# Kernel optimization log

Hardware: AMD Instinct MI355X
Metric: run time of the kernel (lower is better)

Reference implementation:

```python
import jax, jax.numpy as jnp
import numpy as np

B, N, D = 2, 2048, 256
H, HID, EN = 8, 64, 2
ALPHA = 0.2
NEG = -9e15


def setup_inputs() -> dict:
    key = jax.random.key(0)
    k1, k2, k3, k4, k5, k6 = jax.random.split(key, 6)
    fea_mats = jax.random.normal(k1, (B, N, D), dtype=jnp.float32)
    adj_mats = jax.random.randint(k2, (B, N, N), 0, 2).astype(jnp.float32)
    # xavier-uniform-like init (gain 1.414)
    def xav(k, shape):
        fan_in, fan_out = shape[-2], shape[-1]
        bound = 1.414 * np.sqrt(6.0 / (fan_in + fan_out))
        return jax.random.uniform(k, shape, jnp.float32, -bound, bound)
    W_att = xav(k3, (H, D, HID))          # per-head projection
    a_att = xav(k4, (H, 2 * HID, 1))      # per-head attention vector
    W_last = xav(k5, (H * HID, EN))       # last-layer projection
    a_last = xav(k6, (2 * EN, 1))         # last-layer attention vector
    return {"fea_mats": fea_mats, "adj_mats": adj_mats,
            "W_att": W_att, "a_att": a_att,
            "W_last": W_last, "a_last": a_last}


def _leaky(x):
    return jnp.where(x >= 0, x, ALPHA * x)


def _masked_attn(e, adj):
    # torch: where(adj!=0, e, 0) * adj; masked_fill(==0, -9e15); softmax(dim=1 over columns)
    att = jnp.where(adj != 0, e, jnp.zeros_like(e)) * adj
    att = jnp.where(att == 0, jnp.full_like(att, NEG), att)
    return jax.nn.softmax(att, axis=-1)


def reference(fea_mats, adj_mats, W_att, a_att, W_last, a_last):
    # ---- multi-head GAT layers (concat=True), eval mode -> dropout = identity ----
    wh = jnp.einsum('bnd,hdo->bhno', fea_mats, W_att)        # [B,H,N,HID]
    a1 = a_att[:, :HID, 0]                                   # [H,HID]
    a2 = a_att[:, HID:, 0]                                   # [H,HID]
    e1 = jnp.einsum('bhno,ho->bhn', wh, a1)                  # regulon part
    e2 = jnp.einsum('bhno,ho->bhn', wh, a2)                  # gene part
    e = _leaky(e1[:, :, :, None] + e2[:, :, None, :])        # [B,H,N,N]
    att = _masked_attn(e, adj_mats[:, None])                 # [B,H,N,N]
    x = jax.nn.elu(jnp.einsum('bhnm,bhmo->bhno', att, wh))   # [B,H,N,HID]
    x = jnp.transpose(x, (0, 2, 1, 3)).reshape(B, N, H * HID)
    # ---- last layer (concat=False), adj narrowed to square (already square) ----
    wh2 = jnp.einsum('bnd,de->bne', x, W_last)               # [B,N,EN]
    b1 = a_last[:EN, 0]
    b2 = a_last[EN:, 0]
    e = _leaky(jnp.einsum('bne,e->bn', wh2, b1)[:, :, None]
               + jnp.einsum('bne,e->bn', wh2, b2)[:, None, :])  # [B,N,N]
    att = _masked_attn(e, adj_mats)
    out = jax.nn.elu(jnp.einsum('bnm,bme->bne', att, wh2))   # [B,N,EN]
    return out
```

## Files before the change

### kernel.cpp

```cpp
#include <hip/hip_runtime.h>
#include <hip/hip_bf16.h>
#include <cstdint>
#include <cstddef>

#define B_ 2
#define N_ 2048
#define D_ 256
#define H_ 8
#define HID_ 64
#define EN_ 2
#define ALPHA 0.2f
#define NEGBIG (-3.0e38f)
#define LOG2E 1.4426950408889634f

typedef __bf16 bf16x8 __attribute__((ext_vector_type(8)));
typedef float f32x4 __attribute__((ext_vector_type(4)));
typedef unsigned short ushort8 __attribute__((ext_vector_type(8)));
typedef float float4v __attribute__((ext_vector_type(4)));
typedef float float2v __attribute__((ext_vector_type(2)));
typedef unsigned int uint2v __attribute__((ext_vector_type(2)));
typedef unsigned int uint4v __attribute__((ext_vector_type(4)));

__device__ __forceinline__ unsigned short f2bf(float f) {
    unsigned int u = __builtin_bit_cast(unsigned int, f);
    unsigned int r = u + 0x7FFFu + ((u >> 16) & 1u);
    return (unsigned short)(r >> 16);
}
__device__ __forceinline__ float bf2f(unsigned short u) {
    unsigned int x = ((unsigned int)u) << 16;
    return __builtin_bit_cast(float, x);
}
__device__ __forceinline__ float leakyf(float x) { return fmaxf(x, ALPHA * x); }
__device__ __forceinline__ float ub(unsigned int d, int e) {
    return (float)((d >> (8 * e)) & 0xffu);
}

__device__ __forceinline__ ushort8 cvt8(const float* __restrict__ p) {
    float4v x0 = *(const float4v*)p;
    float4v x1 = *(const float4v*)(p + 4);
    ushort8 r;
    #pragma unroll
    for (int e = 0; e < 4; ++e) { r[e] = f2bf(x0[e]); r[e + 4] = f2bf(x1[e]); }
    return r;
}

__global__ __launch_bounds__(256) void k_prep(const float* __restrict__ adj,
                                              unsigned char* __restrict__ adj8) {
    size_t base = ((size_t)blockIdx.x * 256 + threadIdx.x) * 8;
    float4v a = *(const float4v*)(adj + base);
    float4v b = *(const float4v*)(adj + base + 4);
    unsigned int lo = 0, hi = 0;
    #pragma unroll
    for (int e = 0; e < 4; ++e) {
        lo |= (a[e] != 0.f ? 1u : 0u) << (8 * e);
        hi |= (b[e] != 0.f ? 1u : 0u) << (8 * e);
    }
    uint2v o; o[0] = lo; o[1] = hi;
    *(uint2v*)(adj8 + base) = o;
}

__global__ void k_transpose_w(const float* __restrict__ W,
                              unsigned short* __restrict__ WT) {
    int h = blockIdx.x;
    const float* Wh = W + (size_t)h * D_ * HID_;
    unsigned short* WTh = WT + (size_t)h * HID_ * D_;
    for (int idx = threadIdx.x; idx < D_ * HID_; idx += blockDim.x) {
        int d = idx / HID_, o = idx % HID_;
        WTh[o * D_ + d] = f2bf(Wh[idx]);
    }
}

__global__ __launch_bounds__(256) void k_wh(
    const float* __restrict__ fea,
    const unsigned short* __restrict__ WT,
    const float* __restrict__ a_att,
    unsigned short* __restrict__ whT,
    float* __restrict__ e1, float* __restrict__ e2)
{
    int i0 = blockIdx.x << 6;
    int h0 = blockIdx.y * 2;
    int b  = blockIdx.z;

    __shared__ __align__(16) union SmemA {
        struct { unsigned short fa[64 * 72]; unsigned short wt[2][64 * 72]; } s;
        float tr[64 * 65];
    } u;

    int t = threadIdx.x;
    int lane = t & 63;
    int wv = t >> 6;
    int hw = wv & 1;
    int half = wv >> 1;
    int r = lane & 15, q = lane >> 4;
    int ra = t >> 2;
    int cc = (t & 3) * 16;
    int rowbase = half * 32;

    f32x4 acc[2][4] = {};

    const float* fearow = fea + ((size_t)(b * N_ + i0 + ra)) * D_;
    const unsigned short* wt0row = WT + ((size_t)(h0 * 64 + ra)) * D_;
    const unsigned short* wt1row = WT + ((size_t)((h0 + 1) * 64 + ra)) * D_;

    for (int d0 = 0; d0 < D_; d0 += 64) {
        *(ushort8*)&u.s.fa[ra * 72 + cc]       = cvt8(fearow + d0 + cc);
        *(ushort8*)&u.s.fa[ra * 72 + cc + 8]   = cvt8(fearow + d0 + cc + 8);
        *(ushort8*)&u.s.wt[0][ra * 72 + cc]     = *(const ushort8*)(wt0row + d0 + cc);
        *(ushort8*)&u.s.wt[0][ra * 72 + cc + 8] = *(const ushort8*)(wt0row + d0 + cc + 8);
        *(ushort8*)&u.s.wt[1][ra * 72 + cc]     = *(const ushort8*)(wt1row + d0 + cc);
        *(ushort8*)&u.s.wt[1][ra * 72 + cc + 8] = *(const ushort8*)(wt1row + d0 + cc + 8);
        __syncthreads();
        #pragma unroll
        for (int k0 = 0; k0 < 64; k0 += 32) {
            bf16x8 a0 = *(const bf16x8*)&u.s.fa[(rowbase + r) * 72 + k0 + q * 8];
            bf16x8 a1 = *(const bf16x8*)&u.s.fa[(rowbase + 16 + r) * 72 + k0 + q * 8];
            #pragma unroll
            for (int f = 0; f < 4; ++f) {
                bf16x8 bb = *(const bf16x8*)&u.s.wt[hw][(16 * f + r) * 72 + k0 + q * 8];
                acc[0][f] = __builtin_amdgcn_mfma_f32_16x16x32_bf16(a0, bb, acc[0][f], 0, 0, 0);
                acc[1][f] = __builtin_amdgcn_mfma_f32_16x16x32_bf16(a1, bb, acc[1][f], 0, 0, 0);
            }
        }
        __syncthreads();
    }

    float a1v[4], a2v[4];
    #pragma unroll
    for (int f = 0; f < 4; ++f) {
        a1v[f] = a_att[(h0 + hw) * 128 + 16 * f + r];
        a2v[f] = a_att[(h0 + hw) * 128 + 64 + 16 * f + r];
    }
    #pragma unroll
    for (int m = 0; m < 2; ++m) {
        #pragma unroll
        for (int rr = 0; rr < 4; ++rr) {
            float s1 = 0.f, s2 = 0.f;
            #pragma unroll
            for (int f = 0; f < 4; ++f) { s1 += acc[m][f][rr] * a1v[f]; s2 += acc[m][f][rr] * a2v[f]; }
            #pragma unroll
            for (int sh = 1; sh < 16; sh <<= 1) {
                s1 += __shfl_xor(s1, sh, 64);
                s2 += __shfl_xor(s2, sh, 64);
            }
            if (r == 0) {
                int i = i0 + rowbase + 16 * m + 4 * q + rr;
                size_t idx = ((size_t)(b * H_ + h0 + hw)) * N_ + i;
                e1[idx] = s1 * LOG2E; e2[idx] = s2 * LOG2E;
            }
        }
    }

    #pragma unroll
    for (int hh = 0; hh < 2; ++hh) {
        __syncthreads();
        if (hw == hh) {
            #pragma unroll
            for (int m = 0; m < 2; ++m)
                #pragma unroll
                for (int f = 0; f < 4; ++f)
                    #pragma unroll
                    for (int rr = 0; rr < 4; ++rr)
                        u.tr[(16 * f + r) * 65 + rowbase + 16 * m + 4 * q + rr] = acc[m][f][rr];
        }
        __syncthreads();
        {
            int o = t >> 2;
            int ch = (t & 3) * 16;
            unsigned short tmp[16];
            #pragma unroll
            for (int e = 0; e < 16; ++e) tmp[e] = f2bf(u.tr[o * 65 + ch + e]);
            ushort8* dst = (ushort8*)(whT + (((size_t)(b * H_ + h0 + hh) * 64 + o)) * N_ + i0 + ch);
            dst[0] = *(ushort8*)&tmp[0];
            dst[1] = *(ushort8*)&tmp[8];
        }
    }
}

__global__ __launch_bounds__(256) void k_maxe2(const float* __restrict__ e2,
                                               float* __restrict__ mx) {
    int bh = blockIdx.x;
    int t = threadIdx.x;
    const float* row = e2 + (size_t)bh * N_;
    float M = NEGBIG;
    #pragma unroll
    for (int it = 0; it < N_ / 256; ++it) M = fmaxf(M, row[it * 256 + t]);
    #pragma unroll
    for (int s = 1; s < 64; s <<= 1) M = fmaxf(M, __shfl_xor(M, s, 64));
    __shared__ float red[4];
    if ((t & 63) == 0) red[t >> 6] = M;
    __syncthreads();
    if (t == 0) mx[bh] = fmaxf(fmaxf(red[0], red[1]), fmaxf(red[2], red[3]));
}

template<int JPER>
__global__ __launch_bounds__(512, 4) void k_pv2(
    const unsigned char* __restrict__ adj8,
    const unsigned short* __restrict__ whT,
    const float* __restrict__ e1g, const float* __restrict__ e2g,
    const float* __restrict__ maxE2,
    unsigned short* __restrict__ x_part,
    float* __restrict__ zPart)
{
    constexpr int NT = JPER / 64;
    int s  = blockIdx.x;
    int i0 = blockIdx.y << 7;
    int z  = blockIdx.z;
    int b  = z >> 2;
    int h0 = (z & 3) * 2;
    int bh0 = b * H_ + h0;
    int jBeg = s * JPER;

    __shared__ __align__(16) union {
        struct {
            unsigned short wt[2][2][4096];
            unsigned char  adjl[2][128 * 80];
            unsigned int   tv[2][JPER];
        } m;
        unsigned short epi[128][136];
    } u;

    int t = threadIdx.x;
    int lane = t & 63;
    int w = t >> 6;
    int hw = w & 1;
    int rw = (w >> 1) * 32;
    int r = lane & 15, q = lane >> 4;
    int bh = bh0 + hw;

    int ir0 = i0 + rw + r, ir1 = ir0 + 16;
    float mxv = maxE2[bh];
    float e1_0 = e1g[(size_t)bh * N_ + ir0];
    float e1_1 = e1g[(size_t)bh * N_ + ir1];
    float m0 = leakyf(e1_0 + mxv), m1 = leakyf(e1_1 + mxv);
    float sI0 = __builtin_amdgcn_exp2f(e1_0 - m0);
    float uI0 = __builtin_amdgcn_exp2f(ALPHA * e1_0 - m0);
    float sI1 = __builtin_amdgcn_exp2f(e1_1 - m1);
    float uI1 = __builtin_amdgcn_exp2f(ALPHA * e1_1 - m1);

    int sh = t >> 8;
    int so = (t & 255) >> 2;
    int sj = (t & 3) * 16;
    const unsigned short* wsrc = whT + ((size_t)(bh0 + sh) * 64 + so) * N_ + jBeg + sj;
    int wof0 = sh * 4096 + so * 64 + (sj ^ ((so & 7) << 3));
    int wof1 = sh * 4096 + so * 64 + ((sj + 8) ^ ((so & 7) << 3));
    int ar = t >> 2, ac = (t & 3) * 16;
    const unsigned char* asrc = adj8 + ((size_t)(b * N_ + i0 + ar)) * N_ + jBeg + ac;
    int aof = ar * 80 + ac;

    int swzr = (r & 7) << 3;
    int koff0 = (8 * q) ^ swzr;
    int koff1 = (32 + 8 * q) ^ swzr;

    bf16x8 ones;
    #pragma unroll
    for (int e = 0; e < 8; ++e) ones[e] = (__bf16)1.0f;

    f32x4 acc[2][4] = {};
    f32x4 accz[2] = {};

    ushort8 wA, wB;
    uint4v  aR;

#define LOADSTG(tile) do {                                        \
        wA = *(const ushort8*)(wsrc + (tile) * 64);               \
        wB = *(const ushort8*)(wsrc + (tile) * 64 + 8);           \
        aR = *(const uint4v*)(asrc + (tile) * 64);                \
    } while (0)

    for (int jj = t; jj < 2 * JPER; jj += 512) {
        int hh = jj >= JPER ? 1 : 0;
        int j = jj - hh * JPER;
        float ev = e2g[(size_t)(bh0 + hh) * N_ + jBeg + j];
        unsigned int pk = (unsigned int)f2bf(__builtin_amdgcn_exp2f(ev))
                        | ((unsigned int)f2bf(__builtin_amdgcn_exp2f(ALPHA * ev)) << 16);
        u.m.tv[hh][j] = pk;
    }
    LOADSTG(0);
    asm volatile("s_waitcnt vmcnt(0)" ::: "memory");
    *(ushort8*)((unsigned short*)u.m.wt[0] + wof0) = wA;
    *(ushort8*)((unsigned short*)u.m.wt[0] + wof1) = wB;
    *(uint4v*)&u.m.adjl[0][aof] = aR;
    if (NT > 1) LOADSTG(1);
    asm volatile("s_waitcnt lgkmcnt(0)" ::: "memory");
    __builtin_amdgcn_s_barrier();

    #pragma unroll 2
    for (int t8 = 0; t8 < NT; ++t8) {
        const int p = t8 & 1;
        if (t8 + 1 < NT) {
            asm volatile("s_waitcnt vmcnt(0)" ::: "memory");
            *(ushort8*)((unsigned short*)u.m.wt[p ^ 1] + wof0) = wA;
            *(ushort8*)((unsigned short*)u.m.wt[p ^ 1] + wof1) = wB;
            *(uint4v*)&u.m.adjl[p ^ 1][aof] = aR;
        }
        if (t8 + 2 < NT) LOADSTG(t8 + 2);

        const unsigned int* tvp = &u.m.tv[hw][t8 * 64 + q * 8];
        uint4v ta0 = *(const uint4v*)(tvp);
        uint4v ta1 = *(const uint4v*)(tvp + 4);
        uint4v tb0 = *(const uint4v*)(tvp + 32);
        uint4v tb1 = *(const uint4v*)(tvp + 36);
        const unsigned char* ab = &u.m.adjl[p][(rw + r) * 80 + q * 8];
        uint2v a0 = *(const uint2v*)(ab);
        uint2v a1 = *(const uint2v*)(ab + 32);
        uint2v a2 = *(const uint2v*)(ab + 16 * 80);
        uint2v a3 = *(const uint2v*)(ab + 16 * 80 + 32);

        bf16x8 pa00, pa01, pa10, pa11;
        #pragma unroll
        for (int e = 0; e < 4; ++e) {
            float tt, vv;
            unsigned int uu;
            uu = ta0[e];
            tt = __builtin_bit_cast(float, uu << 16);
            vv = __builtin_bit_cast(float, uu & 0xffff0000u);
            pa00[e] = (__bf16)(fmaxf(sI0 * tt, uI0 * vv) * ub(a0[0], e));
            pa10[e] = (__bf16)(fmaxf(sI1 * tt, uI1 * vv) * ub(a2[0], e));
            uu = ta1[e];
            tt = __builtin_bit_cast(float, uu << 16);
            vv = __builtin_bit_cast(float, uu & 0xffff0000u);
            pa00[e + 4] = (__bf16)(fmaxf(sI0 * tt, uI0 * vv) * ub(a0[1], e));
            pa10[e + 4] = (__bf16)(fmaxf(sI1 * tt, uI1 * vv) * ub(a2[1], e));
            uu = tb0[e];
            tt = __builtin_bit_cast(float, uu << 16);
            vv = __builtin_bit_cast(float, uu & 0xffff0000u);
            pa01[e] = (__bf16)(fmaxf(sI0 * tt, uI0 * vv) * ub(a1[0], e));
            pa11[e] = (__bf16)(fmaxf(sI1 * tt, uI1 * vv) * ub(a3[0], e));
            uu = tb1[e];
            tt = __builtin_bit_cast(float, uu << 16);
            vv = __builtin_bit_cast(float, uu & 0xffff0000u);
            pa01[e + 4] = (__bf16)(fmaxf(sI0 * tt, uI0 * vv) * ub(a1[1], e));
            pa11[e + 4] = (__bf16)(fmaxf(sI1 * tt, uI1 * vv) * ub(a3[1], e));
        }

        const unsigned short* Wb = (const unsigned short*)u.m.wt[p] + hw * 4096;
        bf16x8 bb;
        #pragma unroll
        for (int f = 0; f < 4; ++f) {
            bb = *(const bf16x8*)&Wb[f * 1024 + r * 64 + koff0];
            acc[0][f] = __builtin_amdgcn_mfma_f32_16x16x32_bf16(pa00, bb, acc[0][f], 0, 0, 0);
            acc[1][f] = __builtin_amdgcn_mfma_f32_16x16x32_bf16(pa10, bb, acc[1][f], 0, 0, 0);
        }
        accz[0] = __builtin_amdgcn_mfma_f32_16x16x32_bf16(pa00, ones, accz[0], 0, 0, 0);
        accz[1] = __builtin_amdgcn_mfma_f32_16x16x32_bf16(pa10, ones, accz[1], 0, 0, 0);
        #pragma unroll
        for (int f = 0; f < 4; ++f) {
            bb = *(const bf16x8*)&Wb[f * 1024 + r * 64 + koff1];
            acc[0][f] = __builtin_amdgcn_mfma_f32_16x16x32_bf16(pa01, bb, acc[0][f], 0, 0, 0);
            acc[1][f] = __builtin_amdgcn_mfma_f32_16x16x32_bf16(pa11, bb, acc[1][f], 0, 0, 0);
        }
        accz[0] = __builtin_amdgcn_mfma_f32_16x16x32_bf16(pa01, ones, accz[0], 0, 0, 0);
        accz[1] = __builtin_amdgcn_mfma_f32_16x16x32_bf16(pa11, ones, accz[1], 0, 0, 0);

        asm volatile("s_waitcnt lgkmcnt(0)" ::: "memory");
        __builtin_amdgcn_s_barrier();
    }
#undef LOADSTG

    if (r == 0) {
        #pragma unroll
        for (int mR = 0; mR < 2; ++mR)
            #pragma unroll
            for (int rr = 0; rr < 4; ++rr) {
                int i = i0 + rw + mR * 16 + 4 * q + rr;
                zPart[((size_t)(s * 16 + bh)) * N_ + i] = accz[mR][rr];
            }
    }

    #pragma unroll
    for (int mR = 0; mR < 2; ++mR)
        #pragma unroll
        for (int f = 0; f < 4; ++f)
            #pragma unroll
            for (int rr = 0; rr < 4; ++rr)
                u.epi[rw + mR * 16 + 4 * q + rr][hw * 64 + 16 * f + r] = f2bf(acc[mR][f][rr]);
    __syncthreads();
    {
        int tr = t >> 2;
        int ch = (t & 3) * 32;
        const ushort8* src = (const ushort8*)&u.epi[tr][ch];
        ushort8 v0 = src[0], v1 = src[1], v2 = src[2], v3 = src[3];
        unsigned short* dst = x_part
            + ((size_t)s * (B_ * N_) + (size_t)b * N_ + i0 + tr) * 512 + h0 * 64 + ch;
        ((ushort8*)dst)[0] = v0;
        ((ushort8*)dst)[1] = v1;
        ((ushort8*)dst)[2] = v2;
        ((ushort8*)dst)[3] = v3;
    }
}

__global__ __launch_bounds__(256) void k_wh2(
    const unsigned short* __restrict__ x_part,
    const float* __restrict__ zPart,
    const float* __restrict__ W_last,
    const float* __restrict__ a_last,
    float* __restrict__ wh2, float* __restrict__ g1, float* __restrict__ g2,
    int S)
{
    int idx = blockIdx.x * 4 + (threadIdx.x >> 6);
    int lane = threadIdx.x & 63;
    int b = idx >> 11, n = idx & (N_ - 1);
    float a0 = 0.f, a1 = 0.f;
    #pragma unroll
    for (int it = 0; it < 8; ++it) {
        int k = it * 64 + lane;
        float xv = 0.f, zv = 0.f;
        for (int s = 0; s < S; ++s) {
            xv += bf2f(x_part[((size_t)s * (B_ * N_) + idx) * 512 + k]);
            zv += zPart[((size_t)(s * 16 + b * 8 + it)) * N_ + n];
        }
        float x = (zv > 0.f) ? xv / zv : 0.f;
        x = x > 0.f ? x : expm1f(x);
        float2v wl = *(const float2v*)(W_last + k * 2);
        a0 += x * wl[0];
        a1 += x * wl[1];
    }
    #pragma unroll
    for (int s = 1; s < 64; s <<= 1) {
        a0 += __shfl_xor(a0, s, 64);
        a1 += __shfl_xor(a1, s, 64);
    }
    if (lane == 0) {
        wh2[idx * 2] = a0; wh2[idx * 2 + 1] = a1;
        g1[idx] = (a0 * a_last[0] + a1 * a_last[1]) * LOG2E;
        g2[idx] = (a0 * a_last[2] + a1 * a_last[3]) * LOG2E;
    }
}

__global__ __launch_bounds__(256) void k_out(
    const unsigned char* __restrict__ adj8,
    const float* __restrict__ wh2,
    const float* __restrict__ g1, const float* __restrict__ g2,
    float* __restrict__ out)
{
    int idx = blockIdx.x * 4 + (threadIdx.x >> 6);
    int lane = threadIdx.x & 63;
    int b = idx >> 11;
    float gi = g1[idx];
    const unsigned char* arow = adj8 + (size_t)idx * N_;
    const float* g2b = g2 + (size_t)b * N_;
    const float* wh2b = wh2 + (size_t)b * N_ * 2;

    float ep[32];
    float M = NEGBIG;
    #pragma unroll
    for (int it = 0; it < 8; ++it) {
        int j = it * 256 + lane * 4;
        unsigned int d = *(const unsigned int*)(arow + j);
        float4v s4 = *(const float4v*)(g2b + j);
        #pragma unroll
        for (int e = 0; e < 4; ++e) {
            float l = leakyf(gi + s4[e]);
            float v = ((d >> (8 * e)) & 0xffu) ? l : NEGBIG;
            ep[it * 4 + e] = v;
            M = fmaxf(M, v);
        }
    }
    #pragma unroll
    for (int s = 1; s < 64; s <<= 1) M = fmaxf(M, __shfl_xor(M, s, 64));

    float Z = 0.f, A0 = 0.f, A1 = 0.f;
    #pragma unroll
    for (int it = 0; it < 8; ++it) {
        int j = it * 256 + lane * 4;
        float4v wA = *(const float4v*)(wh2b + 2 * j);
        float4v wB = *(const float4v*)(wh2b + 2 * j + 4);
        #pragma unroll
        for (int e = 0; e < 4; ++e) {
            float p = __builtin_amdgcn_exp2f(ep[it * 4 + e] - M);
            Z += p;
            float w0 = (e < 2) ? wA[2 * e] : wB[2 * (e - 2)];
            float w1 = (e < 2) ? wA[2 * e + 1] : wB[2 * (e - 2) + 1];
            A0 += p * w0;
            A1 += p * w1;
        }
    }
    #pragma unroll
    for (int s = 1; s < 64; s <<= 1) {
        Z += __shfl_xor(Z, s, 64);
        A0 += __shfl_xor(A0, s, 64);
        A1 += __shfl_xor(A1, s, 64);
    }
    if (lane == 0) {
        float o0 = A0 / Z, o1 = A1 / Z;
        o0 = o0 > 0.f ? o0 : expm1f(o0);
        o1 = o1 > 0.f ? o1 : expm1f(o1);
        float2v ov; ov[0] = o0; ov[1] = o1;
        *(float2v*)(out + idx * 2) = ov;
    }
}

extern "C" void kernel_launch(void* const* d_in, const int* in_sizes, int n_in,
                              void* d_out, int out_size, void* d_ws, size_t ws_size,
                              hipStream_t stream) {
    const float* fea    = (const float*)d_in[0];
    const float* adj    = (const float*)d_in[1];
    const float* W_att  = (const float*)d_in[2];
    const float* a_att  = (const float*)d_in[3];
    const float* W_last = (const float*)d_in[4];
    const float* a_last = (const float*)d_in[5];

    char* ws = (char*)d_ws;
    float* e1  = (float*)(ws + 0);
    float* e2  = (float*)(ws + 131072);
    float* mxE = (float*)(ws + 262144);
    float* wh2 = (float*)(ws + 262400);
    float* g1  = (float*)(ws + 295168);
    float* g2  = (float*)(ws + 311552);
    unsigned short* WT  = (unsigned short*)(ws + 327936);
    unsigned short* whT = (unsigned short*)(ws + 590080);
    float* zPart = (float*)(ws + 4784384);
    unsigned char* adj8 = (unsigned char*)(ws + 5308672);
    unsigned short* x_part = (unsigned short*)(ws + 13697280);

    const size_t BASE = 13697280ULL, XPART = 4194304ULL;
    int S = (ws_size >= BASE + 2 * XPART) ? 2 : 1;

    k_prep<<<dim3(B_ * N_ * N_ / 2048), dim3(256), 0, stream>>>(adj, adj8);
    k_transpose_w<<<dim3(H_), dim3(256), 0, stream>>>(W_att, WT);
    k_wh<<<dim3(N_ / 64, H_ / 2, B_), dim3(256), 0, stream>>>(
        fea, WT, a_att, whT, e1, e2);
    k_maxe2<<<dim3(B_ * H_), dim3(256), 0, stream>>>(e2, mxE);
    if (S == 2)
        k_pv2<1024><<<dim3(2, N_ / 128, B_ * 4), dim3(512), 0, stream>>>(
            adj8, whT, e1, e2, mxE, x_part, zPart);
    else
        k_pv2<2048><<<dim3(1, N_ / 128, B_ * 4), dim3(512), 0, stream>>>(
            adj8, whT, e1, e2, mxE, x_part, zPart);
    k_wh2<<<dim3(B_ * N_ / 4), dim3(256), 0, stream>>>(
        x_part, zPart, W_last, a_last, wh2, g1, g2, S);
    k_out<<<dim3(B_ * N_ / 4), dim3(256), 0, stream>>>(
        adj8, wh2, g1, g2, (float*)d_out);
}
```

Before: 85.83 us.

## Fuse adjacency prep into projection kernel and compute e2 max via atomics

```diff
diff --git a/kernel.cpp b/kernel.cpp
--- a/kernel.cpp
+++ b/kernel.cpp
@@ -34,6 +34,14 @@
 __device__ __forceinline__ float ub(unsigned int d, int e) {
     return (float)((d >> (8 * e)) & 0xffu);
 }
+__device__ __forceinline__ unsigned fenc(float f) {
+    unsigned b = __builtin_bit_cast(unsigned, f);
+    return (b & 0x80000000u) ? ~b : (b | 0x80000000u);
+}
+__device__ __forceinline__ float fdec(unsigned k) {
+    unsigned b = (k & 0x80000000u) ? (k ^ 0x80000000u) : ~k;
+    return __builtin_bit_cast(float, b);
+}
 
 __device__ __forceinline__ ushort8 cvt8(const float* __restrict__ p) {
     float4v x0 = *(const float4v*)p;
@@ -44,24 +52,11 @@
     return r;
 }
 
-__global__ __launch_bounds__(256) void k_prep(const float* __restrict__ adj,
-                                              unsigned char* __restrict__ adj8) {
-    size_t base = ((size_t)blockIdx.x * 256 + threadIdx.x) * 8;
-    float4v a = *(const float4v*)(adj + base);
-    float4v b = *(const float4v*)(adj + base + 4);
-    unsigned int lo = 0, hi = 0;
-    #pragma unroll
-    for (int e = 0; e < 4; ++e) {
-        lo |= (a[e] != 0.f ? 1u : 0u) << (8 * e);
-        hi |= (b[e] != 0.f ? 1u : 0u) << (8 * e);
-    }
-    uint2v o; o[0] = lo; o[1] = hi;
-    *(uint2v*)(adj8 + base) = o;
-}
-
 __global__ void k_transpose_w(const float* __restrict__ W,
-                              unsigned short* __restrict__ WT) {
+                              unsigned short* __restrict__ WT,
+                              unsigned* __restrict__ mxE) {
     int h = blockIdx.x;
+    if (h == 0 && threadIdx.x < 16) mxE[threadIdx.x] = 0u;
     const float* Wh = W + (size_t)h * D_ * HID_;
     unsigned short* WTh = WT + (size_t)h * HID_ * D_;
     for (int idx = threadIdx.x; idx < D_ * HID_; idx += blockDim.x) {
@@ -70,21 +65,40 @@
     }
 }
 
-__global__ __launch_bounds__(256) void k_wh(
+#define PREP_BLOCKS 4096
+__global__ __launch_bounds__(256) void k_fused1(
+    const float* __restrict__ adj, unsigned char* __restrict__ adj8,
     const float* __restrict__ fea,
     const unsigned short* __restrict__ WT,
     const float* __restrict__ a_att,
     unsigned short* __restrict__ whT,
-    float* __restrict__ e1, float* __restrict__ e2)
+    float* __restrict__ e1, float* __restrict__ e2,
+    unsigned* __restrict__ mxE)
 {
-    int i0 = blockIdx.x << 6;
-    int h0 = blockIdx.y * 2;
-    int b  = blockIdx.z;
-
     __shared__ __align__(16) union SmemA {
         struct { unsigned short fa[64 * 72]; unsigned short wt[2][64 * 72]; } s;
         float tr[64 * 65];
     } u;
+
+    if (blockIdx.x < PREP_BLOCKS) {
+        size_t base = ((size_t)blockIdx.x * 256 + threadIdx.x) * 8;
+        float4v a = *(const float4v*)(adj + base);
+        float4v b = *(const float4v*)(adj + base + 4);
+        unsigned int lo = 0, hi = 0;
+        #pragma unroll
+        for (int e = 0; e < 4; ++e) {
+            lo |= (a[e] != 0.f ? 1u : 0u) << (8 * e);
+            hi |= (b[e] != 0.f ? 1u : 0u) << (8 * e);
+        }
+        uint2v o; o[0] = lo; o[1] = hi;
+        *(uint2v*)(adj8 + base) = o;
+        return;
+    }
+
+    int w = blockIdx.x - PREP_BLOCKS;
+    int i0 = (w & 31) << 6;
+    int h0 = ((w >> 5) & 3) * 2;
+    int b  = w >> 7;
 
     int t = threadIdx.x;
     int lane = t & 63;
@@ -130,6 +144,7 @@
         a1v[f] = a_att[(h0 + hw) * 128 + 16 * f + r];
         a2v[f] = a_att[(h0 + hw) * 128 + 64 + 16 * f + r];
     }
+    float ms2 = NEGBIG;
     #pragma unroll
     for (int m = 0; m < 2; ++m) {
         #pragma unroll
@@ -142,13 +157,18 @@
                 s1 += __shfl_xor(s1, sh, 64);
                 s2 += __shfl_xor(s2, sh, 64);
             }
+            float s2v = s2 * LOG2E;
+            ms2 = fmaxf(ms2, s2v);
             if (r == 0) {
                 int i = i0 + rowbase + 16 * m + 4 * q + rr;
                 size_t idx = ((size_t)(b * H_ + h0 + hw)) * N_ + i;
-                e1[idx] = s1 * LOG2E; e2[idx] = s2 * LOG2E;
+                e1[idx] = s1 * LOG2E; e2[idx] = s2v;
             }
         }
     }
+    ms2 = fmaxf(ms2, __shfl_xor(ms2, 16, 64));
+    ms2 = fmaxf(ms2, __shfl_xor(ms2, 32, 64));
+    if (lane == 0) atomicMax(&mxE[b * H_ + h0 + hw], fenc(ms2));
 
     #pragma unroll
     for (int hh = 0; hh < 2; ++hh) {
@@ -176,28 +196,12 @@
     }
 }
 
-__global__ __launch_bounds__(256) void k_maxe2(const float* __restrict__ e2,
-                                               float* __restrict__ mx) {
-    int bh = blockIdx.x;
-    int t = threadIdx.x;
-    const float* row = e2 + (size_t)bh * N_;
-    float M = NEGBIG;
-    #pragma unroll
-    for (int it = 0; it < N_ / 256; ++it) M = fmaxf(M, row[it * 256 + t]);
-    #pragma unroll
-    for (int s = 1; s < 64; s <<= 1) M = fmaxf(M, __shfl_xor(M, s, 64));
-    __shared__ float red[4];
-    if ((t & 63) == 0) red[t >> 6] = M;
-    __syncthreads();
-    if (t == 0) mx[bh] = fmaxf(fmaxf(red[0], red[1]), fmaxf(red[2], red[3]));
-}
-
 template<int JPER>
 __global__ __launch_bounds__(512, 4) void k_pv2(
     const unsigned char* __restrict__ adj8,
     const unsigned short* __restrict__ whT,
     const float* __restrict__ e1g, const float* __restrict__ e2g,
-    const float* __restrict__ maxE2,
+    const unsigned* __restrict__ maxE2u,
     unsigned short* __restrict__ x_part,
     float* __restrict__ zPart)
 {
@@ -228,7 +232,7 @@
     int bh = bh0 + hw;
 
     int ir0 = i0 + rw + r, ir1 = ir0 + 16;
-    float mxv = maxE2[bh];
+    float mxv = fdec(maxE2u[bh]);
     float e1_0 = e1g[(size_t)bh * N_ + ir0];
     float e1_1 = e1g[(size_t)bh * N_ + ir1];
     float m0 = leakyf(e1_0 + mxv), m1 = leakyf(e1_1 + mxv);
@@ -503,7 +507,7 @@
     char* ws = (char*)d_ws;
     float* e1  = (float*)(ws + 0);
     float* e2  = (float*)(ws + 131072);
-    float* mxE = (float*)(ws + 262144);
+    unsigned* mxE = (unsigned*)(ws + 262144);
     float* wh2 = (float*)(ws + 262400);
     float* g1  = (float*)(ws + 295168);
     float* g2  = (float*)(ws + 311552);
@@ -516,11 +520,9 @@
     const size_t BASE = 13697280ULL, XPART = 4194304ULL;
     int S = (ws_size >= BASE + 2 * XPART) ? 2 : 1;
 
-    k_prep<<<dim3(B_ * N_ * N_ / 2048), dim3(256), 0, stream>>>(adj, adj8);
-    k_transpose_w<<<dim3(H_), dim3(256), 0, stream>>>(W_att, WT);
-    k_wh<<<dim3(N_ / 64, H_ / 2, B_), dim3(256), 0, stream>>>(
-        fea, WT, a_att, whT, e1, e2);
-    k_maxe2<<<dim3(B_ * H_), dim3(256), 0, stream>>>(e2, mxE);
+    k_transpose_w<<<dim3(H_), dim3(256), 0, stream>>>(W_att, WT, mxE);
+    k_fused1<<<dim3(PREP_BLOCKS + 256), dim3(256), 0, stream>>>(
+        adj, adj8, fea, WT, a_att, whT, e1, e2, mxE);
     if (S == 2)
         k_pv2<1024><<<dim3(2, N_ / 128, B_ * 4), dim3(512), 0, stream>>>(
             adj8, whT, e1, e2, mxE, x_part, zPart);
```

Result: slower. 95.98 us (+11.8%).
